# Performance work log

Hardware: AMD Instinct MI355X
Metric: run time of the kernel (lower is better)

Reference implementation:

```python
import jax, jax.numpy as jnp
import numpy as np

B, T, I, H = 512, 1024, 50, 32  # batch, seq_len, input_size, hidden_size


def setup_inputs() -> dict:
    key = jax.random.key(0)
    ks = jax.random.split(key, 13)
    s = 1.0 / np.sqrt(H)  # PyTorch LSTM/Linear uniform init bound

    def u(k, shape):
        return jax.random.uniform(k, shape, jnp.float32, -s, s)

    return {
        "x": jax.random.normal(ks[0], (B, T, I), jnp.float32),
        # forward direction LSTM params (gate order: i, f, g, o)
        "w_ih_f": u(ks[1], (4 * H, I)),
        "w_hh_f": u(ks[2], (4 * H, H)),
        "b_ih_f": u(ks[3], (4 * H,)),
        "b_hh_f": u(ks[4], (4 * H,)),
        # reverse direction LSTM params
        "w_ih_r": u(ks[5], (4 * H, I)),
        "w_hh_r": u(ks[6], (4 * H, H)),
        "b_ih_r": u(ks[7], (4 * H,)),
        "b_hh_r": u(ks[8], (4 * H,)),
        # FC head
        "fc1_w": u(ks[9], (2 * H, 2 * H)),
        "fc1_b": u(ks[10], (2 * H,)),
        "fc3_w": u(ks[11], (1, 2 * H)),
        "fc3_b": u(ks[12], (1,)),
    }


def _lstm_scan(x_proj, w_hh):
    # x_proj: (T, B, 4H) = precomputed input projections + biases
    b = x_proj.shape[1]
    h0 = jnp.zeros((b, H), x_proj.dtype)
    c0 = jnp.zeros((b, H), x_proj.dtype)

    def step(carry, xp):
        h, c = carry
        z = xp + h @ w_hh.T  # (B, 4H)
        i, f, g, o = jnp.split(z, 4, axis=-1)
        c = jax.nn.sigmoid(f) * c + jax.nn.sigmoid(i) * jnp.tanh(g)
        h = jax.nn.sigmoid(o) * jnp.tanh(c)
        return (h, c), h

    _, hs = jax.lax.scan(step, (h0, c0), x_proj)
    return hs  # (T, B, H)


def reference(x, w_ih_f, w_hh_f, b_ih_f, b_hh_f,
              w_ih_r, w_hh_r, b_ih_r, b_hh_r,
              fc1_w, fc1_b, fc3_w, fc3_b):
    xt = jnp.swapaxes(x, 0, 1)  # (T, B, I) time-major for scan
    # batch all input projections up front (big GEMM instead of per-step)
    pf = xt @ w_ih_f.T + (b_ih_f + b_hh_f)          # (T, B, 4H)
    pr = xt[::-1] @ w_ih_r.T + (b_ih_r + b_hh_r)    # reversed time

    hf = _lstm_scan(pf, w_hh_f)           # (T, B, H)
    hr = _lstm_scan(pr, w_hh_r)[::-1]     # flip back to forward time order

    out = jnp.concatenate([hf, hr], axis=-1)  # (T, B, 2H)
    out = jnp.swapaxes(out, 0, 1)             # (B, T, 2H)
    out = out @ fc1_w.T + fc1_b               # fc1
    # dropout(p=0.2) is identity in eval/inference mode
    out = out @ fc3_w.T + fc3_b               # fc3 -> (B, T, 1)
    return out
```

## Files before the change

### kernel.cpp

```cpp
#include <hip/hip_runtime.h>

#define BB 512
#define TT 1024
#define II 50
#define HH 32
#define CH 16
#define NCH (TT / CH)
#define RSLOT 32

typedef float v2f __attribute__((ext_vector_type(2)));
typedef float v4f __attribute__((ext_vector_type(4)));
typedef short v8s __attribute__((ext_vector_type(8)));

__device__ __forceinline__ float fast_rcp(float x) { return __builtin_amdgcn_rcpf(x); }
__device__ __forceinline__ float sigm(float x) { return fast_rcp(1.f + __expf(-x)); }
__device__ __forceinline__ float tanh_(float x) {
    return 1.f - 2.f * fast_rcp(1.f + __expf(2.f * x));
}
__device__ __forceinline__ float hadd(v2f v) { return v.x + v.y; }
__device__ __forceinline__ short bf16rne(float f) {
    unsigned u = __float_as_uint(f);
    u += 0x7FFF + ((u >> 16) & 1);
    return (short)(u >> 16);
}

__global__ void init_out_kernel(float* __restrict__ out,
                                const float* __restrict__ fc1_b,
                                const float* __restrict__ fc3_w,
                                const float* __restrict__ fc3_b,
                                int n) {
    int idx = blockIdx.x * blockDim.x + threadIdx.x;
    float b = fc3_b[0];
    #pragma unroll
    for (int k = 0; k < 64; ++k) b += fc3_w[k] * fc1_b[k];
    if (idx < n) out[idx] = b;
}

__global__ void __launch_bounds__(128, 2) lstm_pc_kernel(
    const float* __restrict__ x,
    const float* __restrict__ w_ih_f, const float* __restrict__ w_hh_f,
    const float* __restrict__ b_ih_f, const float* __restrict__ b_hh_f,
    const float* __restrict__ w_ih_r, const float* __restrict__ w_hh_r,
    const float* __restrict__ b_ih_r, const float* __restrict__ b_hh_r,
    const float* __restrict__ fc1_w, const float* __restrict__ fc3_w,
    float* __restrict__ out)
{
    __shared__ float ringF[RSLOT * 128];
    __shared__ float hbuf[HH][65];
    __shared__ __align__(16) float hst[HH];

    const int tid  = threadIdx.x;
    const int lane = tid & 63;
    const int wave = tid >> 6;
    const int b    = blockIdx.x >> 1;
    const int dir  = blockIdx.x & 1;
    float* outb = out + (size_t)b * TT;

    if (wave == 1) {
        const float* w_ih = dir ? w_ih_r : w_ih_f;
        const float* xb   = x + (size_t)b * TT * II;
        const int nl = lane & 15;
        const int q  = lane >> 4;

        v8s Bf[8][2];
        #pragma unroll
        for (int nt = 0; nt < 8; ++nt) {
            const int n = nt * 16 + nl;
            #pragma unroll
            for (int kf = 0; kf < 2; ++kf)
                #pragma unroll
                for (int j = 0; j < 8; ++j) {
                    const int k = kf * 32 + q * 8 + j;
                    Bf[nt][kf][j] = (k < II) ? bf16rne(w_ih[n * II + k]) : (short)0;
                }
        }

        auto produce_chunk = [&](int c) {
            const int S = c * CH + nl;
            const int t = dir ? (TT - 1 - S) : S;
            const float* xr = xb + (size_t)t * II;
            v8s A0, A1;
            #pragma unroll
            for (int j = 0; j < 8; ++j) A0[j] = bf16rne(xr[q * 8 + j]);
            #pragma unroll
            for (int j = 0; j < 8; ++j) {
                const int k = 32 + q * 8 + j;
                A1[j] = (k < II) ? bf16rne(xr[k]) : (short)0;
            }
            #pragma unroll
            for (int nt = 0; nt < 8; ++nt) {
                v4f acc = {0.f, 0.f, 0.f, 0.f};
                acc = __builtin_amdgcn_mfma_f32_16x16x32_bf16(A0, Bf[nt][0], acc, 0, 0, 0);
                acc = __builtin_amdgcn_mfma_f32_16x16x32_bf16(A1, Bf[nt][1], acc, 0, 0, 0);
                const int nn   = nt * 16 + nl;
                const int cidx = (nn < 64) ? 2 * nn : 2 * (nn - 64) + 1;
                #pragma unroll
                for (int r = 0; r < 4; ++r) {
                    const int slot = (c * CH + q * 4 + r) & (RSLOT - 1);
                    ringF[slot * 128 + cidx] = acc[r];
                }
            }
        };
        auto flush = [&](int m) {
            if (lane < CH) {
                const int ti  = m * CH + lane;
                const int col = ti & 63;
                float d0 = 0.f, d1 = 0.f, d2 = 0.f, d3 = 0.f;
                #pragma unroll
                for (int k = 0; k < HH; k += 4) {
                    d0 += hbuf[k    ][col];
                    d1 += hbuf[k + 1][col];
                    d2 += hbuf[k + 2][col];
                    d3 += hbuf[k + 3][col];
                }
                const int t = dir ? (TT - 1 - ti) : ti;
                atomicAdd(&outb[t], (d0 + d1) + (d2 + d3));
            }
        };

        produce_chunk(0);
        __syncthreads();
        for (int n = 0; n < NCH; ++n) {
            if (n + 1 < NCH) produce_chunk(n + 1);
            if (n >= 1) flush(n - 1);
            __syncthreads();
        }
        flush(NCH - 1);
    } else {
        const float* w_hh = dir ? w_hh_r : w_hh_f;
        const float* bi   = dir ? b_ih_r : b_ih_f;
        const float* bh   = dir ? b_hh_r : b_hh_f;
        v2f whh1p[16], whh2p[16];
        #pragma unroll
        for (int j = 0; j < 16; ++j) {
            whh1p[j].x = w_hh[lane * HH + 2 * j];
            whh1p[j].y = w_hh[lane * HH + 2 * j + 1];
            whh2p[j].x = w_hh[(64 + lane) * HH + 2 * j];
            whh2p[j].y = w_hh[(64 + lane) * HH + 2 * j + 1];
        }
        const float bb1 = bi[lane] + bh[lane];
        const float bb2 = bi[64 + lane] + bh[64 + lane];
        const float M2 = (lane < HH) ? 2.f : 1.f;
        const float A2 = M2;
        const float B2 = (lane < HH) ? -1.f : 0.f;

        float wc = 0.f;
        {
            const int j = dir * HH + (lane & 31);
            #pragma unroll
            for (int n = 0; n < 64; ++n) wc += fc3_w[n] * fc1_w[n * 64 + j];
        }

        if (lane < HH) hst[lane] = 0.f;
        float c = 0.f;

        __syncthreads();

        for (int n = 0; n < NCH; ++n) {
            const int slot0 = (n & 1) * CH;
            const int col0  = (n & 3) * CH;

            v2f xzbuf[CH];
            #pragma unroll
            for (int u = 0; u < CH; ++u)
                xzbuf[u] = *(const v2f*)&ringF[(slot0 + u) * 128 + 2 * lane];

            #pragma unroll
            for (int u = 0; u < CH; ++u) {
                float4 h4[8];
                #pragma unroll
                for (int j = 0; j < 8; ++j) h4[j] = *(const float4*)&hst[4 * j];

                v2f a0 = {bb1, 0.f}, a1 = {0.f, 0.f};
                v2f b0 = {bb2, 0.f}, b1 = {0.f, 0.f};
                #pragma unroll
                for (int j = 0; j < 8; ++j) {
                    v2f p0 = {h4[j].x, h4[j].y};
                    v2f p1 = {h4[j].z, h4[j].w};
                    a0 = __builtin_elementwise_fma(p0, whh1p[2 * j    ], a0);
                    b0 = __builtin_elementwise_fma(p0, whh2p[2 * j    ], b0);
                    a1 = __builtin_elementwise_fma(p1, whh1p[2 * j + 1], a1);
                    b1 = __builtin_elementwise_fma(p1, whh2p[2 * j + 1], b1);
                }
                const v2f xz = xzbuf[u];
                const float z1 = xz.x + hadd(a0 + a1);
                const float z2 = xz.y + hadd(b0 + b1);

                const float g1 = sigm(z1);
                const float g2 = fmaf(A2, sigm(M2 * z2), B2);
                const float p  = g1 * g2;
                const float ph = __shfl_xor(p, 32);

                c = fmaf(g1, c, ph);
                const float h = g2 * tanh_(c);

                if (lane >= HH) {
                    hst[lane - HH] = h;
                    hbuf[lane - HH][col0 + u] = h * wc;
                }
                asm volatile("" ::: "memory");
            }
            __syncthreads();
        }
    }
}

extern "C" void kernel_launch(void* const* d_in, const int* in_sizes, int n_in,
                              void* d_out, int out_size, void* d_ws, size_t ws_size,
                              hipStream_t stream) {
    const float* x      = (const float*)d_in[0];
    const float* w_ih_f = (const float*)d_in[1];
    const float* w_hh_f = (const float*)d_in[2];
    const float* b_ih_f = (const float*)d_in[3];
    const float* b_hh_f = (const float*)d_in[4];
    const float* w_ih_r = (const float*)d_in[5];
    const float* w_hh_r = (const float*)d_in[6];
    const float* b_ih_r = (const float*)d_in[7];
    const float* b_hh_r = (const float*)d_in[8];
    const float* fc1_w  = (const float*)d_in[9];
    const float* fc1_b  = (const float*)d_in[10];
    const float* fc3_w  = (const float*)d_in[11];
    const float* fc3_b  = (const float*)d_in[12];
    float* out = (float*)d_out;

    const int n = BB * TT;
    init_out_kernel<<<(n + 255) / 256, 256, 0, stream>>>(out, fc1_b, fc3_w, fc3_b, n);

    lstm_pc_kernel<<<BB * 2, 128, 0, stream>>>(
        x, w_ih_f, w_hh_f, b_ih_f, b_hh_f,
        w_ih_r, w_hh_r, b_ih_r, b_hh_r,
        fc1_w, fc3_w, out);
}
```

Baseline: 451.4 us.

## Fuse both LSTM directions into one block, one lane per hidden unit

Each block now handles both directions for one batch row. The recurrent wave maps lane to (direction, hidden unit), and each lane computes all four gates itself, so the cross-lane shuffle and the 2x gate-split trick are gone. The producer wave runs the input-projection MFMAs for both directions, writes into a ring buffer twice as wide, and flushes both directions. This halves the grid to 512 blocks and the launch bounds drop to one block per SIMD. The recurrent lane now does twice the FMAs and holds 128 weight registers, and occupancy is lower, in exchange for removing the shuffle dependency on the serial path.

Result: faster. 428.9 us (-5.0%).

```diff
diff --git a/kernel.cpp b/kernel.cpp
--- a/kernel.cpp
+++ b/kernel.cpp
@@ -36,7 +36,7 @@
     if (idx < n) out[idx] = b;
 }
 
-__global__ void __launch_bounds__(128, 2) lstm_pc_kernel(
+__global__ void __launch_bounds__(128, 1) lstm_pc_kernel(
     const float* __restrict__ x,
     const float* __restrict__ w_ih_f, const float* __restrict__ w_hh_f,
     const float* __restrict__ b_ih_f, const float* __restrict__ b_hh_f,
@@ -45,75 +45,88 @@
     const float* __restrict__ fc1_w, const float* __restrict__ fc3_w,
     float* __restrict__ out)
 {
-    __shared__ float ringF[RSLOT * 128];
-    __shared__ float hbuf[HH][65];
-    __shared__ __align__(16) float hst[HH];
+    __shared__ float ringF[RSLOT * 256];
+    __shared__ float hbuf[2][HH][65];
+    __shared__ __align__(16) float hst[64];
 
     const int tid  = threadIdx.x;
     const int lane = tid & 63;
     const int wave = tid >> 6;
-    const int b    = blockIdx.x >> 1;
-    const int dir  = blockIdx.x & 1;
+    const int b    = blockIdx.x;
     float* outb = out + (size_t)b * TT;
 
     if (wave == 1) {
-        const float* w_ih = dir ? w_ih_r : w_ih_f;
-        const float* xb   = x + (size_t)b * TT * II;
+        const float* xb = x + (size_t)b * TT * II;
         const int nl = lane & 15;
         const int q  = lane >> 4;
-
-        v8s Bf[8][2];
+        const float* wih[2] = {w_ih_f, w_ih_r};
+
+        v8s Bf[2][8][2];
         #pragma unroll
-        for (int nt = 0; nt < 8; ++nt) {
-            const int n = nt * 16 + nl;
-            #pragma unroll
-            for (int kf = 0; kf < 2; ++kf)
+        for (int d = 0; d < 2; ++d)
+            #pragma unroll
+            for (int nt = 0; nt < 8; ++nt) {
+                const int n = nt * 16 + nl;
+                #pragma unroll
+                for (int kf = 0; kf < 2; ++kf)
+                    #pragma unroll
+                    for (int j = 0; j < 8; ++j) {
+                        const int k = kf * 32 + q * 8 + j;
+                        Bf[d][nt][kf][j] = (k < II) ? bf16rne(wih[d][n * II + k])
+                                                    : (short)0;
+                    }
+            }
+
+        auto cidx = [](int g) -> int {
+            return (g < 32) ? 2 * g
+                 : (g < 64) ? 2 * (g - 32) + 1
+                 : (g < 96) ? 64 + 2 * (g - 64)
+                            : 64 + 2 * (g - 96) + 1;
+        };
+
+        auto produce_chunk = [&](int c) {
+            #pragma unroll
+            for (int d = 0; d < 2; ++d) {
+                const int S = c * CH + nl;
+                const int t = d ? (TT - 1 - S) : S;
+                const float* xr = xb + (size_t)t * II;
+                v8s A0, A1;
+                #pragma unroll
+                for (int j = 0; j < 8; ++j) A0[j] = bf16rne(xr[q * 8 + j]);
                 #pragma unroll
                 for (int j = 0; j < 8; ++j) {
-                    const int k = kf * 32 + q * 8 + j;
-                    Bf[nt][kf][j] = (k < II) ? bf16rne(w_ih[n * II + k]) : (short)0;
-                }
-        }
-
-        auto produce_chunk = [&](int c) {
-            const int S = c * CH + nl;
-            const int t = dir ? (TT - 1 - S) : S;
-            const float* xr = xb + (size_t)t * II;
-            v8s A0, A1;
-            #pragma unroll
-            for (int j = 0; j < 8; ++j) A0[j] = bf16rne(xr[q * 8 + j]);
-            #pragma unroll
-            for (int j = 0; j < 8; ++j) {
-                const int k = 32 + q * 8 + j;
-                A1[j] = (k < II) ? bf16rne(xr[k]) : (short)0;
-            }
-            #pragma unroll
-            for (int nt = 0; nt < 8; ++nt) {
-                v4f acc = {0.f, 0.f, 0.f, 0.f};
-                acc = __builtin_amdgcn_mfma_f32_16x16x32_bf16(A0, Bf[nt][0], acc, 0, 0, 0);
-                acc = __builtin_amdgcn_mfma_f32_16x16x32_bf16(A1, Bf[nt][1], acc, 0, 0, 0);
-                const int nn   = nt * 16 + nl;
-                const int cidx = (nn < 64) ? 2 * nn : 2 * (nn - 64) + 1;
-                #pragma unroll
-                for (int r = 0; r < 4; ++r) {
-                    const int slot = (c * CH + q * 4 + r) & (RSLOT - 1);
-                    ringF[slot * 128 + cidx] = acc[r];
+                    const int k = 32 + q * 8 + j;
+                    A1[j] = (k < II) ? bf16rne(xr[k]) : (short)0;
+                }
+                #pragma unroll
+                for (int nt = 0; nt < 8; ++nt) {
+                    v4f acc = {0.f, 0.f, 0.f, 0.f};
+                    acc = __builtin_amdgcn_mfma_f32_16x16x32_bf16(A0, Bf[d][nt][0], acc, 0, 0, 0);
+                    acc = __builtin_amdgcn_mfma_f32_16x16x32_bf16(A1, Bf[d][nt][1], acc, 0, 0, 0);
+                    const int col = d * 128 + cidx(nt * 16 + nl);
+                    #pragma unroll
+                    for (int r = 0; r < 4; ++r) {
+                        const int slot = (c * CH + q * 4 + r) & (RSLOT - 1);
+                        ringF[slot * 256 + col] = acc[r];
+                    }
                 }
             }
         };
         auto flush = [&](int m) {
-            if (lane < CH) {
-                const int ti  = m * CH + lane;
+            if (lane < 32) {
+                const int d   = lane >> 4;
+                const int idx = lane & 15;
+                const int ti  = m * CH + idx;
                 const int col = ti & 63;
                 float d0 = 0.f, d1 = 0.f, d2 = 0.f, d3 = 0.f;
                 #pragma unroll
                 for (int k = 0; k < HH; k += 4) {
-                    d0 += hbuf[k    ][col];
-                    d1 += hbuf[k + 1][col];
-                    d2 += hbuf[k + 2][col];
-                    d3 += hbuf[k + 3][col];
-                }
-                const int t = dir ? (TT - 1 - ti) : ti;
+                    d0 += hbuf[d][k    ][col];
+                    d1 += hbuf[d][k + 1][col];
+                    d2 += hbuf[d][k + 2][col];
+                    d3 += hbuf[d][k + 3][col];
+                }
+                const int t = d ? (TT - 1 - ti) : ti;
                 atomicAdd(&outb[t], (d0 + d1) + (d2 + d3));
             }
         };
@@ -127,31 +140,33 @@
         }
         flush(NCH - 1);
     } else {
-        const float* w_hh = dir ? w_hh_r : w_hh_f;
-        const float* bi   = dir ? b_ih_r : b_ih_f;
-        const float* bh   = dir ? b_hh_r : b_hh_f;
-        v2f whh1p[16], whh2p[16];
+        const int d = lane >> 5;
+        const int k = lane & 31;
+        const float* w_hh = d ? w_hh_r : w_hh_f;
+        const float* bi   = d ? b_ih_r : b_ih_f;
+        const float* bh   = d ? b_hh_r : b_hh_f;
+
+        v2f wp[4][16];
+        float bb[4];
         #pragma unroll
-        for (int j = 0; j < 16; ++j) {
-            whh1p[j].x = w_hh[lane * HH + 2 * j];
-            whh1p[j].y = w_hh[lane * HH + 2 * j + 1];
-            whh2p[j].x = w_hh[(64 + lane) * HH + 2 * j];
-            whh2p[j].y = w_hh[(64 + lane) * HH + 2 * j + 1];
-        }
-        const float bb1 = bi[lane] + bh[lane];
-        const float bb2 = bi[64 + lane] + bh[64 + lane];
-        const float M2 = (lane < HH) ? 2.f : 1.f;
-        const float A2 = M2;
-        const float B2 = (lane < HH) ? -1.f : 0.f;
+        for (int D = 0; D < 4; ++D) {
+            const int row = D * 32 + k;
+            #pragma unroll
+            for (int j = 0; j < 16; ++j) {
+                wp[D][j].x = w_hh[row * HH + 2 * j];
+                wp[D][j].y = w_hh[row * HH + 2 * j + 1];
+            }
+            bb[D] = bi[row] + bh[row];
+        }
 
         float wc = 0.f;
         {
-            const int j = dir * HH + (lane & 31);
+            const int j = d * HH + k;
             #pragma unroll
             for (int n = 0; n < 64; ++n) wc += fc3_w[n] * fc1_w[n * 64 + j];
         }
 
-        if (lane < HH) hst[lane] = 0.f;
+        hst[lane] = 0.f;
         float c = 0.f;
 
         __syncthreads();
@@ -159,45 +174,48 @@
         for (int n = 0; n < NCH; ++n) {
             const int slot0 = (n & 1) * CH;
             const int col0  = (n & 3) * CH;
-
-            v2f xzbuf[CH];
-            #pragma unroll
-            for (int u = 0; u < CH; ++u)
-                xzbuf[u] = *(const v2f*)&ringF[(slot0 + u) * 128 + 2 * lane];
-
             #pragma unroll
             for (int u = 0; u < CH; ++u) {
+                const float* rp = &ringF[(slot0 + u) * 256 + d * 128 + 2 * k];
+                const v2f xz1 = *(const v2f*)rp;
+                const v2f xz2 = *(const v2f*)(rp + 64);
+
                 float4 h4[8];
                 #pragma unroll
-                for (int j = 0; j < 8; ++j) h4[j] = *(const float4*)&hst[4 * j];
-
-                v2f a0 = {bb1, 0.f}, a1 = {0.f, 0.f};
-                v2f b0 = {bb2, 0.f}, b1 = {0.f, 0.f};
+                for (int j = 0; j < 8; ++j)
+                    h4[j] = *(const float4*)&hst[d * 32 + 4 * j];
+
+                v2f aA[4], aB[4];
+                #pragma unroll
+                for (int D = 0; D < 4; ++D) {
+                    aA[D] = (v2f){bb[D], 0.f};
+                    aB[D] = (v2f){0.f, 0.f};
+                }
                 #pragma unroll
                 for (int j = 0; j < 8; ++j) {
                     v2f p0 = {h4[j].x, h4[j].y};
                     v2f p1 = {h4[j].z, h4[j].w};
-                    a0 = __builtin_elementwise_fma(p0, whh1p[2 * j    ], a0);
-                    b0 = __builtin_elementwise_fma(p0, whh2p[2 * j    ], b0);
-                    a1 = __builtin_elementwise_fma(p1, whh1p[2 * j + 1], a1);
-                    b1 = __builtin_elementwise_fma(p1, whh2p[2 * j + 1], b1);
-                }
-                const v2f xz = xzbuf[u];
-                const float z1 = xz.x + hadd(a0 + a1);
-                const float z2 = xz.y + hadd(b0 + b1);
-
-                const float g1 = sigm(z1);
-                const float g2 = fmaf(A2, sigm(M2 * z2), B2);
-                const float p  = g1 * g2;
-                const float ph = __shfl_xor(p, 32);
-
-                c = fmaf(g1, c, ph);
-                const float h = g2 * tanh_(c);
-
-                if (lane >= HH) {
-                    hst[lane - HH] = h;
-                    hbuf[lane - HH][col0 + u] = h * wc;
-                }
+                    #pragma unroll
+                    for (int D = 0; D < 4; ++D) {
+                        aA[D] = __builtin_elementwise_fma(p0, wp[D][2 * j    ], aA[D]);
+                        aB[D] = __builtin_elementwise_fma(p1, wp[D][2 * j + 1], aB[D]);
+                    }
+                }
+                const float zi = xz1.x + hadd(aA[0] + aB[0]);
+                const float zf = xz1.y + hadd(aA[1] + aB[1]);
+                const float zg = xz2.x + hadd(aA[2] + aB[2]);
+                const float zo = xz2.y + hadd(aA[3] + aB[3]);
+
+                const float gi = sigm(zi);
+                const float gf = sigm(zf);
+                const float gg = tanh_(zg);
+                const float go = sigm(zo);
+
+                c = fmaf(gf, c, gi * gg);
+                const float h = go * tanh_(c);
+
+                hst[lane] = h;
+                hbuf[d][k][col0 + u] = h * wc;
                 asm volatile("" ::: "memory");
             }
             __syncthreads();
@@ -226,7 +244,7 @@
     const int n = BB * TT;
     init_out_kernel<<<(n + 255) / 256, 256, 0, stream>>>(out, fc1_b, fc3_w, fc3_b, n);
 
-    lstm_pc_kernel<<<BB * 2, 128, 0, stream>>>(
+    lstm_pc_kernel<<<BB, 128, 0, stream>>>(
         x, w_ih_f, w_hh_f, b_ih_f, b_hh_f,
         w_ih_r, w_hh_r, b_ih_r, b_hh_r,
         fc1_w, fc3_w, out);
```
